# Performance work log

Measured on AMD Instinct MI355X. Metric: run time of the kernel, lower is better.

## Reference

```python
import jax, jax.numpy as jnp
import numpy as np

NEG_INF = -1e30  # stand-in for float('-inf'); safe under softmax


def setup_inputs() -> dict:
    key = jax.random.key(0)
    k0, k1, k2, k3 = jax.random.split(key, 4)
    B, T, C, H = 8, 2048, 1024, 64
    x = jax.random.normal(k0, (B, T, C), dtype=jnp.float32)
    Wq = jax.random.normal(k1, (C, H), dtype=jnp.float32) * (C ** -0.5)
    Wk = jax.random.normal(k2, (C, H), dtype=jnp.float32) * (C ** -0.5)
    Wv = jax.random.normal(k3, (C, H), dtype=jnp.float32) * (C ** -0.5)
    return {"x": x, "Wq": Wq, "Wk": Wk, "Wv": Wv}


def reference(x, Wq, Wk, Wv):
    # x: [B, T, C]; projections (no bias): [B, T, H]
    B, T, C = x.shape
    q = jnp.einsum('btc,ch->bth', x, Wq)
    k = jnp.einsum('btc,ch->bth', x, Wk)
    v = jnp.einsum('btc,ch->bth', x, Wv)
    # raw scores (NOTE: original applies NO 1/sqrt(head_size) scaling)
    scores = jnp.einsum('bth,bsh->bts', q, k)  # [B, T, T]
    causal = jnp.tril(jnp.ones((T, T), dtype=bool))
    scores = jnp.where(causal[None, :, :], scores, NEG_INF)
    # NOTE: original uses softmax over dim=1 (query axis), kept faithfully.
    attn = jax.nn.softmax(scores, axis=1)
    # dropout is identity in eval mode
    return jnp.einsum('bts,bsh->bth', attn, v)  # [B, T, H]
```

## Files before the change

kernel.cpp:

```cpp
#include <hip/hip_runtime.h>
#include <hip/hip_bf16.h>

#define BB 8
#define TT 2048
#define CC 1024
#define HH 64
#define NTRI 528
#define NPB (TT * HH)

typedef unsigned short ushort_t;
typedef __attribute__((ext_vector_type(8))) short bf16x8;
typedef __attribute__((ext_vector_type(4))) float f32x4;

__device__ __forceinline__ float bf2f(ushort_t u) {
    unsigned int x = ((unsigned int)u) << 16;
    return __uint_as_float(x);
}
__device__ __forceinline__ ushort_t f2bf(float f) {
    unsigned int x = __float_as_uint(f);
    unsigned int lsb = (x >> 16) & 1;
    x += 0x7fffu + lsb;
    return (ushort_t)(x >> 16);
}

__global__ __launch_bounds__(256) void wsplit_kernel(
    const float* __restrict__ Wq, const float* __restrict__ Wk,
    const float* __restrict__ Wv, ushort_t* __restrict__ wpack)
{
    int slot = blockIdx.x * 256 + threadIdx.x;
    int rec = slot >> 6, lane = slot & 63;
    int quad = lane >> 4, l15 = lane & 15;
    int part = rec >> 7;
    int r2 = rec & 127;
    int kc = r2 >> 2, nt = r2 & 3;
    const float* W = (part < 2) ? Wq : (part < 4) ? Wk : Wv;
    bool lo = (part < 4) && (part & 1);
    bf16x8 o;
    #pragma unroll
    for (int j = 0; j < 8; j++) {
        int c = kc * 32 + quad * 8 + j;
        float w = W[(size_t)c * HH + nt * 16 + l15];
        ushort_t h = f2bf(w);
        o[j] = (short)(lo ? f2bf(w - bf2f(h)) : h);
    }
    *(bf16x8*)(wpack + (size_t)rec * 512 + lane * 8) = o;
}

__global__ __launch_bounds__(256) void proj_mfma(
    const float* __restrict__ x, const ushort_t* __restrict__ wpack,
    ushort_t* __restrict__ qpk, ushort_t* __restrict__ qpl,
    ushort_t* __restrict__ kpk, ushort_t* __restrict__ kpl,
    ushort_t* __restrict__ vpk)
{
    const int tid = threadIdx.x;
    const int lane = tid & 63, wid = tid >> 6;
    const int quad = lane >> 4, l15 = lane & 15;
    const int r0 = blockIdx.x * 32;
    const int mtW = wid >> 1, ntH = wid & 1;
    const int nt0 = ntH * 2;

    __shared__ __align__(16) unsigned char smem[3 * 32 * 72 * 4];
    ushort_t* xh = (ushort_t*)smem;
    ushort_t* xl = (ushort_t*)(smem + 32 * 72 * 2);
    float* sC = (float*)smem;

    f32x4 acc[3][2];
    #pragma unroll
    for (int p = 0; p < 3; p++)
        #pragma unroll
        for (int g = 0; g < 2; g++)
            acc[p][g] = (f32x4){0.f, 0.f, 0.f, 0.f};

    float4 cur[2];
    #pragma unroll
    for (int i = 0; i < 2; i++) {
        int slot = tid + i * 256;
        int row = slot >> 4, c4 = (slot & 15) * 4;
        cur[i] = *(const float4*)(x + (size_t)(r0 + row) * CC + c4);
    }

    for (int bk = 0; bk < 16; bk++) {
        if (bk) __syncthreads();
        #pragma unroll
        for (int i = 0; i < 2; i++) {
            int slot = tid + i * 256;
            int row = slot >> 4, c4 = (slot & 15) * 4;
            float vv[4] = {cur[i].x, cur[i].y, cur[i].z, cur[i].w};
            ushort4 h4, l4;
            ushort_t* hp = (ushort_t*)&h4;
            ushort_t* lp = (ushort_t*)&l4;
            #pragma unroll
            for (int j = 0; j < 4; j++) {
                ushort_t h = f2bf(vv[j]);
                hp[j] = h;
                lp[j] = f2bf(vv[j] - bf2f(h));
            }
            *(ushort4*)(xh + row * 72 + c4) = h4;
            *(ushort4*)(xl + row * 72 + c4) = l4;
        }
        __syncthreads();
        if (bk < 15) {
            #pragma unroll
            for (int i = 0; i < 2; i++) {
                int slot = tid + i * 256;
                int row = slot >> 4, c4 = (slot & 15) * 4;
                cur[i] = *(const float4*)(x + (size_t)(r0 + row) * CC + (bk + 1) * 64 + c4);
            }
        }
        #pragma unroll
        for (int c = 0; c < 2; c++) {
            const int kc = bk * 2 + c;
            bf16x8 aH = *(const bf16x8*)(xh + (mtW * 16 + l15) * 72 + c * 32 + quad * 8);
            bf16x8 aL = *(const bf16x8*)(xl + (mtW * 16 + l15) * 72 + c * 32 + quad * 8);
            #pragma unroll
            for (int g = 0; g < 2; g++) {
                const int nt = nt0 + g;
                const size_t lb8 = (size_t)lane * 8;
                bf16x8 bQh = *(const bf16x8*)(wpack + (((size_t)(0 * 32 + kc) * 4 + nt) * 512) + lb8);
                bf16x8 bQl = *(const bf16x8*)(wpack + (((size_t)(1 * 32 + kc) * 4 + nt) * 512) + lb8);
                bf16x8 bKh = *(const bf16x8*)(wpack + (((size_t)(2 * 32 + kc) * 4 + nt) * 512) + lb8);
                bf16x8 bKl = *(const bf16x8*)(wpack + (((size_t)(3 * 32 + kc) * 4 + nt) * 512) + lb8);
                bf16x8 bVh = *(const bf16x8*)(wpack + (((size_t)(4 * 32 + kc) * 4 + nt) * 512) + lb8);
                acc[0][g] = __builtin_amdgcn_mfma_f32_16x16x32_bf16(aL, bQh, acc[0][g], 0, 0, 0);
                acc[0][g] = __builtin_amdgcn_mfma_f32_16x16x32_bf16(aH, bQl, acc[0][g], 0, 0, 0);
                acc[0][g] = __builtin_amdgcn_mfma_f32_16x16x32_bf16(aH, bQh, acc[0][g], 0, 0, 0);
                acc[1][g] = __builtin_amdgcn_mfma_f32_16x16x32_bf16(aL, bKh, acc[1][g], 0, 0, 0);
                acc[1][g] = __builtin_amdgcn_mfma_f32_16x16x32_bf16(aH, bKl, acc[1][g], 0, 0, 0);
                acc[1][g] = __builtin_amdgcn_mfma_f32_16x16x32_bf16(aH, bKh, acc[1][g], 0, 0, 0);
                acc[2][g] = __builtin_amdgcn_mfma_f32_16x16x32_bf16(aH, bVh, acc[2][g], 0, 0, 0);
            }
        }
    }
    __syncthreads();

    #pragma unroll
    for (int p = 0; p < 3; p++)
        #pragma unroll
        for (int g = 0; g < 2; g++) {
            const int nt = nt0 + g;
            #pragma unroll
            for (int r = 0; r < 4; r++)
                sC[(p * 32 + mtW * 16 + quad * 4 + r) * 72 + nt * 16 + l15] = acc[p][g][r];
        }
    __syncthreads();

    const int b = r0 >> 11;
    {
        const int rec = tid >> 6;
        const int mtR = rec >> 1, ksR = rec & 1;
        const int gt = ((r0 & 2047) >> 4) + mtR;
        const size_t dst = (size_t)b * NPB + (((size_t)ksR * 128 + gt) * 64 + lane) * 8;
        #pragma unroll
        for (int p = 0; p < 2; p++) {
            const float* src = &sC[(p * 32 + mtR * 16 + l15) * 72 + ksR * 32 + quad * 8];
            f32x4 v0 = *(const f32x4*)src;
            f32x4 v1 = *(const f32x4*)(src + 4);
            bf16x8 h8, l8;
            #pragma unroll
            for (int j = 0; j < 4; j++) {
                ushort_t h = f2bf(v0[j]);
                h8[j] = (short)h;
                l8[j] = (short)f2bf(v0[j] - bf2f(h));
            }
            #pragma unroll
            for (int j = 0; j < 4; j++) {
                ushort_t h = f2bf(v1[j]);
                h8[4 + j] = (short)h;
                l8[4 + j] = (short)f2bf(v1[j] - bf2f(h));
            }
            *(bf16x8*)((p == 0 ? qpk : kpk) + dst) = h8;
            *(bf16x8*)((p == 0 ? qpl : kpl) + dst) = l8;
        }
    }
    {
        const int nt = tid >> 6;
        const int scL = (r0 & 2047) >> 5;
        bf16x8 o;
        #pragma unroll
        for (int j = 0; j < 8; j++)
            o[j] = (short)f2bf(sC[(2 * 32 + quad * 8 + j) * 72 + nt * 16 + l15]);
        *(bf16x8*)(vpk + (size_t)b * NPB + (((size_t)scL * 4 + nt) * 64 + lane) * 8) = o;
    }
}

__global__ __launch_bounds__(256) void colsum_mfma(
    const ushort_t* __restrict__ qpk, const ushort_t* __restrict__ qpl,
    const ushort_t* __restrict__ kpk, const ushort_t* __restrict__ kpl,
    float* __restrict__ lsum, ushort_t* __restrict__ Ppack)
{
    const int tc = blockIdx.x, st = blockIdx.y, b = blockIdx.z;
    if (tc < st) return;
    const int tid = threadIdx.x;
    const int lane = tid & 63, wid = tid >> 6;
    const int quad = lane >> 4, l15 = lane & 15;
    const int wy = wid >> 1, wx = wid & 1;
    const int t_base = tc * 128 + wy * 64;
    const int s_base = st * 128 + wx * 64;
    if (t_base < s_base) return;
    const bool needMask = (t_base == s_base);

    __shared__ __align__(16) ushort_t sT[4][64][72];

    const size_t bq = (size_t)b * NPB;
    const size_t lb8 = (size_t)lane * 8;

    bf16x8 bH[4][2], bL[4][2];
    #pragma unroll
    for (int nt = 0; nt < 4; nt++)
        #pragma unroll
        for (int ks = 0; ks < 2; ks++) {
            const size_t off = bq + (((size_t)ks * 128 + (s_base >> 4) + nt) * 64) * 8 + lb8;
            bH[nt][ks] = *(const bf16x8*)(kpk + off);
            bL[nt][ks] = *(const bf16x8*)(kpl + off);
        }

    float cs[4] = {0.f, 0.f, 0.f, 0.f};

    #pragma unroll
    for (int mt = 0; mt < 4; mt++) {
        bf16x8 aH[2], aL[2];
        #pragma unroll
        for (int ks = 0; ks < 2; ks++) {
            const size_t off = bq + (((size_t)ks * 128 + (t_base >> 4) + mt) * 64) * 8 + lb8;
            aH[ks] = *(const bf16x8*)(qpk + off);
            aL[ks] = *(const bf16x8*)(qpl + off);
        }
        f32x4 acc[4];
        #pragma unroll
        for (int nt = 0; nt < 4; nt++)
            acc[nt] = (f32x4){0.f, 0.f, 0.f, 0.f};
        #pragma unroll
        for (int nt = 0; nt < 4; nt++)
            #pragma unroll
            for (int ks = 0; ks < 2; ks++) {
                acc[nt] = __builtin_amdgcn_mfma_f32_16x16x32_bf16(aL[ks], bH[nt][ks], acc[nt], 0, 0, 0);
                acc[nt] = __builtin_amdgcn_mfma_f32_16x16x32_bf16(aH[ks], bL[nt][ks], acc[nt], 0, 0, 0);
                acc[nt] = __builtin_amdgcn_mfma_f32_16x16x32_bf16(aH[ks], bH[nt][ks], acc[nt], 0, 0, 0);
            }
        #pragma unroll
        for (int nt = 0; nt < 4; nt++)
            #pragma unroll
            for (int r = 0; r < 4; r++) {
                float e = __expf(acc[nt][r]);
                if (needMask) {
                    int t = mt * 16 + quad * 4 + r;
                    int s = nt * 16 + l15;
                    if (t < s) e = 0.f;
                }
                cs[nt] += e;
                sT[wid][mt * 16 + quad * 4 + r][nt * 16 + l15] = f2bf(e);
            }
    }

    #pragma unroll
    for (int nt = 0; nt < 4; nt++) {
        float v = cs[nt];
        v += __shfl_xor(v, 16);
        v += __shfl_xor(v, 32);
        if (quad == 0)
            atomicAdd(lsum + (size_t)b * TT + s_base + nt * 16 + l15, v);
    }

    const int ti = t_base >> 6, si = s_base >> 6;
    ushort_t* tp = Ppack + ((size_t)b * NTRI + (size_t)(ti * (ti + 1) / 2) + si) * 4096;
    #pragma unroll
    for (int rec = 0; rec < 8; rec++) {
        const int mtP = rec >> 1, ksP = rec & 1;
        bf16x8 v8 = *(const bf16x8*)&sT[wid][mtP * 16 + l15][ksP * 32 + quad * 8];
        *(bf16x8*)(tp + (size_t)rec * 512 + lb8) = v8;
    }
}

__global__ __launch_bounds__(256) void vscale_kernel(
    const ushort_t* __restrict__ vpk, const float* __restrict__ lsum,
    ushort_t* __restrict__ vps)
{
    size_t slot = (size_t)blockIdx.x * 256 + threadIdx.x;
    int lane = (int)(slot & 63);
    int quad = lane >> 4;
    int sc_b = (int)(slot >> 8);
    int b = sc_b >> 6, sc = sc_b & 63;
    bf16x8 in = *(const bf16x8*)(vpk + slot * 8);
    const float* lp = lsum + (size_t)b * TT + sc * 32 + quad * 8;
    float4 l0 = *(const float4*)lp;
    float4 l1 = *(const float4*)(lp + 4);
    float li[8] = {l0.x, l0.y, l0.z, l0.w, l1.x, l1.y, l1.z, l1.w};
    bf16x8 o;
    #pragma unroll
    for (int j = 0; j < 8; j++)
        o[j] = (short)f2bf(bf2f((ushort_t)in[j]) / li[j]);
    *(bf16x8*)(vps + slot * 8) = o;
}

__global__ __launch_bounds__(256) void attn_pv(
    const ushort_t* __restrict__ Ppack, const ushort_t* __restrict__ vps,
    float* __restrict__ out)
{
    const int p = blockIdx.x, b = blockIdx.y;
    const int tid = threadIdx.x;
    const int lane = tid & 63, wid = tid >> 6;
    const int quad = lane >> 4, l15 = lane & 15;
    const size_t lb8 = (size_t)lane * 8;

    __shared__ __align__(16) float red[4][2048];

    const ushort_t* vb_ = vps + (size_t)b * NPB;

    #pragma unroll
    for (int half = 0; half < 2; half++) {
        const int tileI = half ? (63 - p) : p;
        const int t0 = tileI * 32;
        const int ti = t0 >> 6, trel16 = (t0 & 63) >> 4;
        const size_t triBase = ((size_t)b * NTRI + (size_t)(ti * (ti + 1) / 2)) * 4096;

        f32x4 oacc[2][4];
        #pragma unroll
        for (int mt = 0; mt < 2; mt++)
            #pragma unroll
            for (int nt = 0; nt < 4; nt++)
                oacc[mt][nt] = (f32x4){0.f, 0.f, 0.f, 0.f};

        for (int s0 = wid * 64; s0 <= t0 + 31; s0 += 256) {
            const int si = s0 >> 6;
            const ushort_t* tp = Ppack + triBase + (size_t)si * 4096;
            bf16x8 pa[2][2];
            #pragma unroll
            for (int mt = 0; mt < 2; mt++)
                #pragma unroll
                for (int ks = 0; ks < 2; ks++)
                    pa[mt][ks] = *(const bf16x8*)(tp + (size_t)((trel16 + mt) * 2 + ks) * 512 + lb8);
            #pragma unroll
            for (int ks = 0; ks < 2; ks++)
                #pragma unroll
                for (int nt = 0; nt < 4; nt++) {
                    bf16x8 vb = *(const bf16x8*)(vb_ + (((size_t)(s0 >> 5) + ks) * 4 + nt) * 512 + lb8);
                    #pragma unroll
                    for (int mt = 0; mt < 2; mt++)
                        oacc[mt][nt] = __builtin_amdgcn_mfma_f32_16x16x32_bf16(pa[mt][ks], vb, oacc[mt][nt], 0, 0, 0);
                }
        }

        __syncthreads();
        #pragma unroll
        for (int mt = 0; mt < 2; mt++)
            #pragma unroll
            for (int nt = 0; nt < 4; nt++)
                #pragma unroll
                for (int r = 0; r < 4; r++)
                    red[wid][(mt * 16 + quad * 4 + r) * 64 + nt * 16 + l15] =
                        oacc[mt][nt][r];
        __syncthreads();
        for (int e = tid; e < 2048; e += 256) {
            float s_ = red[0][e] + red[1][e] + red[2][e] + red[3][e];
            out[(size_t)(b * TT + t0 + (e >> 6)) * HH + (e & 63)] = s_;
        }
        __syncthreads();
    }
}

extern "C" void kernel_launch(void* const* d_in, const int* in_sizes, int n_in,
                              void* d_out, int out_size, void* d_ws, size_t ws_size,
                              hipStream_t stream)
{
    const float* x  = (const float*)d_in[0];
    const float* Wq = (const float*)d_in[1];
    const float* Wk = (const float*)d_in[2];
    const float* Wv = (const float*)d_in[3];
    float* out = (float*)d_out;

    const size_t N = (size_t)BB * TT * HH;
    ushort_t* qpk = (ushort_t*)d_ws;
    ushort_t* qpl = qpk + N;
    ushort_t* kpk = qpl + N;
    ushort_t* kpl = kpk + N;
    ushort_t* vpk = kpl + N;
    ushort_t* vps = vpk + N;
    float* lsum = (float*)(vps + N);
    ushort_t* wpack = (ushort_t*)(lsum + (size_t)BB * TT);
    ushort_t* Ppack = wpack + (size_t)5 * 32 * 4 * 512;

    hipMemsetAsync(lsum, 0, (size_t)BB * TT * sizeof(float), stream);
    wsplit_kernel<<<dim3(160), 256, 0, stream>>>(Wq, Wk, Wv, wpack);
    proj_mfma<<<dim3(512), 256, 0, stream>>>(x, wpack, qpk, qpl, kpk, kpl, vpk);
    colsum_mfma<<<dim3(16, 16, BB), 256, 0, stream>>>(qpk, qpl, kpk, kpl, lsum, Ppack);
    vscale_kernel<<<dim3(512), 256, 0, stream>>>(vpk, lsum, vps);
    attn_pv<<<dim3(32, BB), 256, 0, stream>>>(Ppack, vps, out);
}
```

Before: 168.5 us.

## Halve projection row tile and double-buffer x staging in shared memory

The projection kernel now handles 16 rows per block instead of 32, so the grid grows from 512 to 1024 blocks and each wave owns one 16-column tile. The x staging buffer is double-buffered in shared memory, which drops one barrier per K step. This raises parallelism across CUs, but each block's wpack weight reads are now shared by only 16 rows, doubling total weight traffic. The V pack write is restricted to the half of the 32-row group that the block owns.

```diff
diff --git a/kernel.cpp b/kernel.cpp
--- a/kernel.cpp
+++ b/kernel.cpp
@@ -55,37 +55,29 @@
     const int tid = threadIdx.x;
     const int lane = tid & 63, wid = tid >> 6;
     const int quad = lane >> 4, l15 = lane & 15;
-    const int r0 = blockIdx.x * 32;
-    const int mtW = wid >> 1, ntH = wid & 1;
-    const int nt0 = ntH * 2;
-
-    __shared__ __align__(16) unsigned char smem[3 * 32 * 72 * 4];
-    ushort_t* xh = (ushort_t*)smem;
-    ushort_t* xl = (ushort_t*)(smem + 32 * 72 * 2);
-    float* sC = (float*)smem;
-
-    f32x4 acc[3][2];
+    const int r0 = blockIdx.x * 16;
+    const int nt = wid;
+
+    __shared__ __align__(16) ushort_t xh[2][16][72];
+    __shared__ __align__(16) ushort_t xl[2][16][72];
+    __shared__ __align__(16) float sC[3][16][72];
+
+    f32x4 acc[3];
     #pragma unroll
     for (int p = 0; p < 3; p++)
-        #pragma unroll
-        for (int g = 0; g < 2; g++)
-            acc[p][g] = (f32x4){0.f, 0.f, 0.f, 0.f};
-
-    float4 cur[2];
-    #pragma unroll
-    for (int i = 0; i < 2; i++) {
-        int slot = tid + i * 256;
-        int row = slot >> 4, c4 = (slot & 15) * 4;
-        cur[i] = *(const float4*)(x + (size_t)(r0 + row) * CC + c4);
-    }
+        acc[p] = (f32x4){0.f, 0.f, 0.f, 0.f};
+
+    const int srow = tid >> 4, sc4 = (tid & 15) * 4;
+    const float* xrow = x + (size_t)(r0 + srow) * CC + sc4;
+
+    float4 cur = *(const float4*)xrow;
+
+    const size_t lb8 = (size_t)lane * 8;
 
     for (int bk = 0; bk < 16; bk++) {
-        if (bk) __syncthreads();
-        #pragma unroll
-        for (int i = 0; i < 2; i++) {
-            int slot = tid + i * 256;
-            int row = slot >> 4, c4 = (slot & 15) * 4;
-            float vv[4] = {cur[i].x, cur[i].y, cur[i].z, cur[i].w};
+        const int buf = bk & 1;
+        {
+            float vv[4] = {cur.x, cur.y, cur.z, cur.w};
             ushort4 h4, l4;
             ushort_t* hp = (ushort_t*)&h4;
             ushort_t* lp = (ushort_t*)&l4;
@@ -95,91 +87,76 @@
                 hp[j] = h;
                 lp[j] = f2bf(vv[j] - bf2f(h));
             }
-            *(ushort4*)(xh + row * 72 + c4) = h4;
-            *(ushort4*)(xl + row * 72 + c4) = l4;
+            *(ushort4*)(&xh[buf][srow][sc4]) = h4;
+            *(ushort4*)(&xl[buf][srow][sc4]) = l4;
         }
         __syncthreads();
-        if (bk < 15) {
-            #pragma unroll
-            for (int i = 0; i < 2; i++) {
-                int slot = tid + i * 256;
-                int row = slot >> 4, c4 = (slot & 15) * 4;
-                cur[i] = *(const float4*)(x + (size_t)(r0 + row) * CC + (bk + 1) * 64 + c4);
-            }
-        }
+        if (bk < 15)
+            cur = *(const float4*)(xrow + (bk + 1) * 64);
+
         #pragma unroll
         for (int c = 0; c < 2; c++) {
             const int kc = bk * 2 + c;
-            bf16x8 aH = *(const bf16x8*)(xh + (mtW * 16 + l15) * 72 + c * 32 + quad * 8);
-            bf16x8 aL = *(const bf16x8*)(xl + (mtW * 16 + l15) * 72 + c * 32 + quad * 8);
-            #pragma unroll
-            for (int g = 0; g < 2; g++) {
-                const int nt = nt0 + g;
-                const size_t lb8 = (size_t)lane * 8;
-                bf16x8 bQh = *(const bf16x8*)(wpack + (((size_t)(0 * 32 + kc) * 4 + nt) * 512) + lb8);
-                bf16x8 bQl = *(const bf16x8*)(wpack + (((size_t)(1 * 32 + kc) * 4 + nt) * 512) + lb8);
-                bf16x8 bKh = *(const bf16x8*)(wpack + (((size_t)(2 * 32 + kc) * 4 + nt) * 512) + lb8);
-                bf16x8 bKl = *(const bf16x8*)(wpack + (((size_t)(3 * 32 + kc) * 4 + nt) * 512) + lb8);
-                bf16x8 bVh = *(const bf16x8*)(wpack + (((size_t)(4 * 32 + kc) * 4 + nt) * 512) + lb8);
-                acc[0][g] = __builtin_amdgcn_mfma_f32_16x16x32_bf16(aL, bQh, acc[0][g], 0, 0, 0);
-                acc[0][g] = __builtin_amdgcn_mfma_f32_16x16x32_bf16(aH, bQl, acc[0][g], 0, 0, 0);
-                acc[0][g] = __builtin_amdgcn_mfma_f32_16x16x32_bf16(aH, bQh, acc[0][g], 0, 0, 0);
-                acc[1][g] = __builtin_amdgcn_mfma_f32_16x16x32_bf16(aL, bKh, acc[1][g], 0, 0, 0);
-                acc[1][g] = __builtin_amdgcn_mfma_f32_16x16x32_bf16(aH, bKl, acc[1][g], 0, 0, 0);
-                acc[1][g] = __builtin_amdgcn_mfma_f32_16x16x32_bf16(aH, bKh, acc[1][g], 0, 0, 0);
-                acc[2][g] = __builtin_amdgcn_mfma_f32_16x16x32_bf16(aH, bVh, acc[2][g], 0, 0, 0);
-            }
-        }
-    }
+            bf16x8 aH = *(const bf16x8*)(&xh[buf][l15][c * 32 + quad * 8]);
+            bf16x8 aL = *(const bf16x8*)(&xl[buf][l15][c * 32 + quad * 8]);
+            bf16x8 bQh = *(const bf16x8*)(wpack + (((size_t)(0 * 32 + kc) * 4 + nt) * 512) + lb8);
+            bf16x8 bQl = *(const bf16x8*)(wpack + (((size_t)(1 * 32 + kc) * 4 + nt) * 512) + lb8);
+            bf16x8 bKh = *(const bf16x8*)(wpack + (((size_t)(2 * 32 + kc) * 4 + nt) * 512) + lb8);
+            bf16x8 bKl = *(const bf16x8*)(wpack + (((size_t)(3 * 32 + kc) * 4 + nt) * 512) + lb8);
+            bf16x8 bVh = *(const bf16x8*)(wpack + (((size_t)(4 * 32 + kc) * 4 + nt) * 512) + lb8);
+            acc[0] = __builtin_amdgcn_mfma_f32_16x16x32_bf16(aL, bQh, acc[0], 0, 0, 0);
+            acc[0] = __builtin_amdgcn_mfma_f32_16x16x32_bf16(aH, bQl, acc[0], 0, 0, 0);
+            acc[0] = __builtin_amdgcn_mfma_f32_16x16x32_bf16(aH, bQh, acc[0], 0, 0, 0);
+            acc[1] = __builtin_amdgcn_mfma_f32_16x16x32_bf16(aL, bKh, acc[1], 0, 0, 0);
+            acc[1] = __builtin_amdgcn_mfma_f32_16x16x32_bf16(aH, bKl, acc[1], 0, 0, 0);
+            acc[1] = __builtin_amdgcn_mfma_f32_16x16x32_bf16(aH, bKh, acc[1], 0, 0, 0);
+            acc[2] = __builtin_amdgcn_mfma_f32_16x16x32_bf16(aH, bVh, acc[2], 0, 0, 0);
+        }
+    }
+
+    #pragma unroll
+    for (int p = 0; p < 3; p++)
+        #pragma unroll
+        for (int r = 0; r < 4; r++)
+            sC[p][quad * 4 + r][nt * 16 + l15] = acc[p][r];
     __syncthreads();
 
-    #pragma unroll
-    for (int p = 0; p < 3; p++)
-        #pragma unroll
-        for (int g = 0; g < 2; g++) {
-            const int nt = nt0 + g;
-            #pragma unroll
-            for (int r = 0; r < 4; r++)
-                sC[(p * 32 + mtW * 16 + quad * 4 + r) * 72 + nt * 16 + l15] = acc[p][g][r];
-        }
-    __syncthreads();
-
     const int b = r0 >> 11;
+    const int gt = (r0 & 2047) >> 4;
+
     {
-        const int rec = tid >> 6;
-        const int mtR = rec >> 1, ksR = rec & 1;
-        const int gt = ((r0 & 2047) >> 4) + mtR;
+        const int rec = wid;
+        const int p = rec >> 1, ksR = rec & 1;
         const size_t dst = (size_t)b * NPB + (((size_t)ksR * 128 + gt) * 64 + lane) * 8;
-        #pragma unroll
-        for (int p = 0; p < 2; p++) {
-            const float* src = &sC[(p * 32 + mtR * 16 + l15) * 72 + ksR * 32 + quad * 8];
-            f32x4 v0 = *(const f32x4*)src;
-            f32x4 v1 = *(const f32x4*)(src + 4);
-            bf16x8 h8, l8;
-            #pragma unroll
-            for (int j = 0; j < 4; j++) {
-                ushort_t h = f2bf(v0[j]);
-                h8[j] = (short)h;
-                l8[j] = (short)f2bf(v0[j] - bf2f(h));
-            }
-            #pragma unroll
-            for (int j = 0; j < 4; j++) {
-                ushort_t h = f2bf(v1[j]);
-                h8[4 + j] = (short)h;
-                l8[4 + j] = (short)f2bf(v1[j] - bf2f(h));
-            }
-            *(bf16x8*)((p == 0 ? qpk : kpk) + dst) = h8;
-            *(bf16x8*)((p == 0 ? qpl : kpl) + dst) = l8;
-        }
+        const float* src = &sC[p][l15][ksR * 32 + quad * 8];
+        f32x4 v0 = *(const f32x4*)src;
+        f32x4 v1 = *(const f32x4*)(src + 4);
+        bf16x8 h8, l8;
+        #pragma unroll
+        for (int j = 0; j < 4; j++) {
+            ushort_t h = f2bf(v0[j]);
+            h8[j] = (short)h;
+            l8[j] = (short)f2bf(v0[j] - bf2f(h));
+        }
+        #pragma unroll
+        for (int j = 0; j < 4; j++) {
+            ushort_t h = f2bf(v1[j]);
+            h8[4 + j] = (short)h;
+            l8[4 + j] = (short)f2bf(v1[j] - bf2f(h));
+        }
+        *(bf16x8*)((p == 0 ? qpk : kpk) + dst) = h8;
+        *(bf16x8*)((p == 0 ? qpl : kpl) + dst) = l8;
     }
     {
-        const int nt = tid >> 6;
         const int scL = (r0 & 2047) >> 5;
-        bf16x8 o;
-        #pragma unroll
-        for (int j = 0; j < 8; j++)
-            o[j] = (short)f2bf(sC[(2 * 32 + quad * 8 + j) * 72 + nt * 16 + l15]);
-        *(bf16x8*)(vpk + (size_t)b * NPB + (((size_t)scL * 4 + nt) * 64 + lane) * 8) = o;
+        const int half = (r0 >> 4) & 1;
+        if ((quad >> 1) == half) {
+            bf16x8 o;
+            #pragma unroll
+            for (int j = 0; j < 8; j++)
+                o[j] = (short)f2bf(sC[2][(quad & 1) * 8 + j][nt * 16 + l15]);
+            *(bf16x8*)(vpk + (size_t)b * NPB + (((size_t)scL * 4 + nt) * 64 + lane) * 8) = o;
+        }
     }
 }
 
@@ -381,7 +358,7 @@
 
     hipMemsetAsync(lsum, 0, (size_t)BB * TT * sizeof(float), stream);
     wsplit_kernel<<<dim3(160), 256, 0, stream>>>(Wq, Wk, Wv, wpack);
-    proj_mfma<<<dim3(512), 256, 0, stream>>>(x, wpack, qpk, qpl, kpk, kpl, vpk);
+    proj_mfma<<<dim3(1024), 256, 0, stream>>>(x, wpack, qpk, qpl, kpk, kpl, vpk);
     colsum_mfma<<<dim3(16, 16, BB), 256, 0, stream>>>(qpk, qpl, kpk, kpl, lsum, Ppack);
     vscale_kernel<<<dim3(512), 256, 0, stream>>>(vpk, lsum, vps);
     attn_pv<<<dim3(32, BB), 256, 0, stream>>>(Ppack, vps, out);
```

Result: no change. 171.2 us (+1.6%).
